# Kernel tuning notes

Measured on AMD Instinct MI355X. Metric: run time of the kernel, lower is better.

The kernel has to match this reference:

```python
import jax, jax.numpy as jnp
import numpy as np

B, SQ, SK, D = 8, 2048, 768, 768  # SK must equal D for layer_combine concat to typecheck


def setup_inputs() -> dict:
    key = jax.random.key(0)
    ks = jax.random.split(key, 13)
    s = 0.02
    return {
        "query": jax.random.normal(ks[0], (B, SQ, D), jnp.float32),
        "key_matrix": jax.random.normal(ks[1], (B, SK, D), jnp.float32),
        "value_matrix": jax.random.normal(ks[2], (B, SK, D), jnp.float32),
        "prev_layer": jax.random.normal(ks[3], (SK, D), jnp.float32) * s,
        "attention_mask": jax.random.randint(ks[4], (B, 1, SK), 0, 2, jnp.int32),
        "Wq": jax.random.normal(ks[5], (D, D), jnp.float32) * s,
        "bq": jax.random.normal(ks[6], (D,), jnp.float32) * s,
        "Wk": jax.random.normal(ks[7], (D, D), jnp.float32) * s,
        "bk": jax.random.normal(ks[8], (D,), jnp.float32) * s,
        "Wv": jax.random.normal(ks[9], (D, D), jnp.float32) * s,
        "bv": jax.random.normal(ks[10], (D,), jnp.float32) * s,
        "Wc": jax.random.normal(ks[11], (D, 2 * D), jnp.float32) * s,
        "bc": jax.random.normal(ks[12], (D,), jnp.float32) * s,
    }


def reference(query, key_matrix, value_matrix, prev_layer, attention_mask,
              Wq, bq, Wk, bk, Wv, bv, Wc, bc):
    # Linear projections (torch Linear: x @ W.T + b)
    Q = query @ Wq.T + bq                      # [B, SQ, D]
    K = key_matrix @ Wk.T + bk                 # [B, SK, D]
    V = value_matrix @ Wv.T + bv               # computed but unused when prev_layer given (faithful)
    scale = 1.0 / np.sqrt(D).astype(np.float32)
    scores = jnp.einsum('bqd,bkd->bqk', Q, K) * scale  # [B, SQ, SK]
    scores = jnp.where(attention_mask == 0, jnp.float32(-1e9), scores)
    # prev-layer integration: matmul + concat + linear combine
    layer_attn = scores @ prev_layer           # [B, SQ, D]
    combined = jnp.concatenate([scores, layer_attn], axis=-1)  # [B, SQ, 2D]
    out = combined @ Wc.T + bc                 # [B, SQ, D]
    return out
```

## Files before the change

### kernel.cpp

```cpp
#include <hip/hip_runtime.h>
#include <hip/hip_bf16.h>


typedef __attribute__((ext_vector_type(8))) short short8;
typedef __attribute__((ext_vector_type(4))) float f32x4;

#define SCALE 0.03608439182435161f

__device__ inline unsigned short f2bf(float x) {
  unsigned int u = __builtin_bit_cast(unsigned int, x);
  u = (u + 0x7fffu + ((u >> 16) & 1u)) >> 16;
  return (unsigned short)u;
}
__device__ inline float bf2f(unsigned short h) {
  return __builtin_bit_cast(float, ((unsigned int)h) << 16);
}

__global__ void k_cvt(const float* __restrict__ s, unsigned short* __restrict__ d, int n4) {
  int i = blockIdx.x * 256 + threadIdx.x;
  if (i >= n4) return;
  float4 v = reinterpret_cast<const float4*>(s)[i];
  reinterpret_cast<ushort4*>(d)[i] = make_ushort4(f2bf(v.x), f2bf(v.y), f2bf(v.z), f2bf(v.w));
}

__global__ void k_prep(const float* __restrict__ prev, const float* __restrict__ Wc,
                       unsigned short* __restrict__ prev_bf,
                       unsigned short* __restrict__ Wc2_bf) {
  int g = blockIdx.x;
  int region = g / 576;
  int idx = (g - region * 576) * 256 + threadIdx.x;
  float4 v;
  unsigned short* dst;
  if (region == 0) { v = reinterpret_cast<const float4*>(prev)[idx]; dst = prev_bf; }
  else {
    int r = idx / 192, c4 = (idx - r * 192) * 4;
    v = *reinterpret_cast<const float4*>(Wc + (long long)r * 1536 + 768 + c4);
    dst = Wc2_bf;
  }
  reinterpret_cast<ushort4*>(dst)[idx] = make_ushort4(f2bf(v.x), f2bf(v.y), f2bf(v.z), f2bf(v.w));
}

__global__ void k_tcvt(const float* __restrict__ Wq, const float* __restrict__ Wk,
                       const float* __restrict__ key, const int* __restrict__ mask,
                       unsigned short* __restrict__ WqT, unsigned short* __restrict__ WkT,
                       unsigned short* __restrict__ keyzT) {
  __shared__ float t[64][65];
  int z = blockIdx.z;
  const float* src;
  unsigned short* dst;
  const int* mb = nullptr;
  if (z == 0) { src = Wq; dst = WqT; }
  else if (z == 1) { src = Wk; dst = WkT; }
  else {
    int b = z - 2;
    src = key + (long long)b * 589824;
    dst = keyzT + (long long)b * 589824;
    mb = mask + b * 768;
  }
  int bx = blockIdx.x * 64, by = blockIdx.y * 64;
  int tx = threadIdx.x & 63, ty = threadIdx.x >> 6;
  #pragma unroll
  for (int i = 0; i < 64; i += 4) {
    float v = src[(long long)(by + ty + i) * 768 + bx + tx];
    if (mb) v = mb[by + ty + i] ? v : 0.0f;
    t[ty + i][tx] = v;
  }
  __syncthreads();
  #pragma unroll
  for (int i = 0; i < 64; i += 4)
    dst[(long long)(bx + ty + i) * 768 + by + tx] = f2bf(t[tx][ty + i]);
}

__global__ void k_sums(const unsigned short* __restrict__ WqT,
                       const unsigned short* __restrict__ WkT,
                       const float* __restrict__ bk, const float* __restrict__ bq,
                       const float* __restrict__ Mt, const int* __restrict__ mask,
                       float* __restrict__ u, float* __restrict__ w3,
                       float* __restrict__ s1, float* __restrict__ sm0) {
  int gw = blockIdx.x * 4 + (threadIdx.x >> 6);
  int lane = threadIdx.x & 63;
  if (gw < 1536) {
    const unsigned short* wrow = (gw < 768) ? (WqT + (long long)gw * 768)
                                            : (WkT + (long long)(gw - 768) * 768);
    const float* vec = (gw < 768) ? bk : bq;
    float s = 0.f;
    for (int j = lane; j < 768; j += 64) s += bf2f(wrow[j]) * vec[j];
    #pragma unroll
    for (int off = 32; off > 0; off >>= 1) s += __shfl_down(s, off, 64);
    if (lane == 0) { if (gw < 768) u[gw] = s; else w3[gw - 768] = s; }
  } else {
    int g2 = gw - 1536;
    int b = g2 / 768, d2 = g2 - b * 768;
    if (b >= 8) return;
    const int* mb = mask + b * 768;
    const float* mrow = Mt + (long long)d2 * 768;
    float a1 = 0.f, a0 = 0.f;
    for (int k = lane; k < 768; k += 64) {
      float v = mrow[k];
      if (mb[k]) a1 += v; else a0 += v;
    }
    #pragma unroll
    for (int off = 32; off > 0; off >>= 1) {
      a1 += __shfl_down(a1, off, 64);
      a0 += __shfl_down(a0, off, 64);
    }
    if (lane == 0) { s1[g2] = a1; sm0[g2] = a0; }
  }
}

__global__ void k_row(const unsigned short* __restrict__ Tt, const float* __restrict__ w3,
                      const float* __restrict__ s1, const float* __restrict__ sm0,
                      const float* __restrict__ bq, const float* __restrict__ bk,
                      const float* __restrict__ bc, float* __restrict__ row) {
  int gw = blockIdx.x * 4 + (threadIdx.x >> 6);
  int lane = threadIdx.x & 63;
  int b = gw / 768, d2 = gw - b * 768;
  if (b >= 8) return;
  const unsigned short* trow = Tt + ((long long)b * 768 + d2) * 768;
  float st = 0.f, sbb = 0.f;
  for (int j = lane; j < 768; j += 64) {
    st += bf2f(trow[j]) * w3[j];
    sbb += bq[j] * bk[j];
  }
  #pragma unroll
  for (int off = 32; off > 0; off >>= 1) {
    st += __shfl_down(st, off, 64);
    sbb += __shfl_down(sbb, off, 64);
  }
  if (lane == 0)
    row[gw] = bc[d2] - 1e9f * sm0[gw] + SCALE * (st + sbb * s1[gw]);
}

template <int MODE>
__global__ __launch_bounds__(256) void gemm_nt(
    const unsigned short* __restrict__ A, long long aStr, int lda,
    const unsigned short* __restrict__ B, long long bStr, int ldb,
    float* __restrict__ Cf, unsigned short* __restrict__ Cbf,
    long long cStr, int ldc,
    const float* __restrict__ aux, const float* __restrict__ aux2)
{
  constexpr int BM = 64, BN = 64, BK = 64;
  __shared__ __align__(16) char As[BM * BK * 2];
  __shared__ __align__(16) char Bs[BN * BK * 2];

  const int gx = gridDim.x, gy = gridDim.y;
  const int nwg = gx * gy * (int)gridDim.z;
  int lin = blockIdx.x + gx * (blockIdx.y + gy * blockIdx.z);
  int qq = nwg >> 3, rr = nwg & 7, xcd = lin & 7, loc = lin >> 3;
  int swz = (xcd < rr ? xcd * (qq + 1) : rr * (qq + 1) + (xcd - rr) * qq) + loc;
  int bz = swz / (gx * gy);
  int rem = swz - bz * gx * gy;
  int by = rem / gx, bx = rem - by * gx;

  const int b = bz;
  const unsigned short* Ab = A + (long long)b * aStr;
  const unsigned short* Bb = B + (long long)b * bStr;
  const int m0 = by * BM, n0 = bx * BN;

  const int tid = threadIdx.x;
  const int w = tid >> 6, lane = tid & 63;
  const int wr = w >> 1, wc = w & 1;
  const int fr = lane & 15, fq = lane >> 4;

  f32x4 acc[2][2] = {};

  for (int kt = 0; kt < 768; kt += BK) {
    __syncthreads();
    #pragma unroll
    for (int t = 0; t < 2; ++t) {
      int g = t * 256 + tid;
      int row = g >> 3, s = g & 7;
      int sg = (s - row) & 7;
      const unsigned short* ga = Ab + (long long)(m0 + row) * lda + kt + sg * 8;
      __builtin_amdgcn_global_load_lds(
          (const __attribute__((address_space(1))) void*)ga,
          (__attribute__((address_space(3))) void*)(As + g * 16), 16, 0, 0);
    }
    #pragma unroll
    for (int t = 0; t < 2; ++t) {
      int g = t * 256 + tid;
      int row = g >> 3, s = g & 7;
      int sg = (s - row) & 7;
      const unsigned short* gb = Bb + (long long)(n0 + row) * ldb + kt + sg * 8;
      __builtin_amdgcn_global_load_lds(
          (const __attribute__((address_space(1))) void*)gb,
          (__attribute__((address_space(3))) void*)(Bs + g * 16), 16, 0, 0);
    }
    __syncthreads();

    #pragma unroll
    for (int kk = 0; kk < 2; ++kk) {
      short8 af[2], bfr[2];
      #pragma unroll
      for (int i = 0; i < 2; ++i) {
        int r = wr * 32 + i * 16 + fr;
        int sgi = ((kk * 4 + fq) + r) & 7;
        af[i] = *reinterpret_cast<const short8*>(As + r * 128 + sgi * 16);
      }
      #pragma unroll
      for (int j = 0; j < 2; ++j) {
        int r = wc * 32 + j * 16 + fr;
        int sgj = ((kk * 4 + fq) + r) & 7;
        bfr[j] = *reinterpret_cast<const short8*>(Bs + r * 128 + sgj * 16);
      }
      #pragma unroll
      for (int i = 0; i < 2; ++i)
        #pragma unroll
        for (int j = 0; j < 2; ++j)
          acc[i][j] = __builtin_amdgcn_mfma_f32_16x16x32_bf16(af[i], bfr[j], acc[i][j], 0, 0, 0);
    }
  }

  #pragma unroll
  for (int i = 0; i < 2; ++i)
    #pragma unroll
    for (int j = 0; j < 2; ++j)
      #pragma unroll
      for (int r = 0; r < 4; ++r) {
        int row = m0 + wr * 32 + i * 16 + fq * 4 + r;
        int col = n0 + wc * 32 + j * 16 + fr;
        float v = acc[i][j][r];
        if constexpr (MODE == 0) {
          v += aux[(long long)row * 1536 + col];
          Cf[(long long)row * 768 + col] = v;
          Cbf[(long long)row * 768 + col] = f2bf(v);
        } else if constexpr (MODE == 2) {
          Cbf[(long long)b * cStr + (long long)row * ldc + col] = f2bf(v);
        } else {
          v += aux[b * 768 + row] * aux2[col];
          Cbf[(long long)b * cStr + (long long)row * ldc + col] = f2bf(v);
        }
      }
}

__global__ __launch_bounds__(512, 1) void g5_pipe(
    const unsigned short* __restrict__ A,
    const unsigned short* __restrict__ B,
    float* __restrict__ C, const float* __restrict__ rowv)
{
  __shared__ __align__(16) char As[2][256 * 128];
  __shared__ __align__(16) char Bs[2][192 * 128];

  int lin = blockIdx.x + 4 * (blockIdx.y + 8 * blockIdx.z);
  int swz = (lin & 7) * 32 + (lin >> 3);
  int bz = swz >> 5;
  int rem = swz & 31;
  int by = rem >> 2, bx = rem & 3;

  const int b = bz;
  const int m0 = by * 256, n0 = bx * 192;
  const unsigned short* Ab = A + (long long)b * 1572864;
  const unsigned short* Bb = B + (long long)b * 589824;

  const int tid = threadIdx.x;
  const int w = tid >> 6, lane = tid & 63;
  const int wr = w >> 2, wn = w & 3;
  const int fr = lane & 15, fq = lane >> 4;

  f32x4 acc[8][3] = {};

  auto stageA = [&](int buf, int kt, int s0, int ns) {
    for (int s = s0; s < s0 + ns; ++s) {
      int g = s * 512 + tid;
      int row = g >> 3, slot = g & 7;
      int sg = (slot - row) & 7;
      const unsigned short* ga = Ab + (long long)(m0 + row) * 768 + kt + sg * 8;
      __builtin_amdgcn_global_load_lds(
          (const __attribute__((address_space(1))) void*)ga,
          (__attribute__((address_space(3))) void*)(&As[buf][0] + g * 16), 16, 0, 0);
    }
  };
  auto stageB = [&](int buf, int kt, int s0, int ns) {
    for (int s = s0; s < s0 + ns; ++s) {
      int g = s * 512 + tid;
      int row = g >> 3, slot = g & 7;
      int sg = (slot - row) & 7;
      const unsigned short* gb = Bb + (long long)(n0 + row) * 768 + kt + sg * 8;
      __builtin_amdgcn_global_load_lds(
          (const __attribute__((address_space(1))) void*)gb,
          (__attribute__((address_space(3))) void*)(&Bs[buf][0] + g * 16), 16, 0, 0);
    }
  };

  stageA(0, 0, 0, 4);
  stageB(0, 0, 0, 3);
  asm volatile("s_waitcnt vmcnt(0)" ::: "memory");
  __builtin_amdgcn_s_barrier();
  __builtin_amdgcn_sched_barrier(0);

  int cur = 0;
  for (int t = 0; t < 12; ++t) {
    const char* as = &As[cur][0];
    const char* bs = &Bs[cur][0];
    const int ktn = (t + 1) * 64;
    short8 a0[4], a1[4], bb[3];

    #pragma unroll
    for (int i = 0; i < 4; ++i) {
      int r = wr * 128 + i * 16 + fr;
      a0[i] = *reinterpret_cast<const short8*>(as + r * 128 + (((fq) + r) & 7) * 16);
    }
    #pragma unroll
    for (int j = 0; j < 3; ++j) {
      int r = wn * 48 + j * 16 + fr;
      bb[j] = *reinterpret_cast<const short8*>(bs + r * 128 + (((fq) + r) & 7) * 16);
    }
    if (t < 11) stageA(cur ^ 1, ktn, 0, 2);
    __builtin_amdgcn_s_barrier();
    __builtin_amdgcn_s_setprio(1);
    #pragma unroll
    for (int i = 0; i < 4; ++i)
      #pragma unroll
      for (int j = 0; j < 3; ++j)
        acc[i][j] = __builtin_amdgcn_mfma_f32_16x16x32_bf16(a0[i], bb[j], acc[i][j], 0, 0, 0);
    __builtin_amdgcn_s_setprio(0);
    __builtin_amdgcn_s_barrier();

    #pragma unroll
    for (int i = 0; i < 4; ++i) {
      int r = wr * 128 + (4 + i) * 16 + fr;
      a1[i] = *reinterpret_cast<const short8*>(as + r * 128 + (((fq) + r) & 7) * 16);
    }
    if (t < 11) { stageA(cur ^ 1, ktn, 2, 2); stageB(cur ^ 1, ktn, 0, 1); }
    __builtin_amdgcn_s_barrier();
    __builtin_amdgcn_s_setprio(1);
    #pragma unroll
    for (int i = 0; i < 4; ++i)
      #pragma unroll
      for (int j = 0; j < 3; ++j)
        acc[4 + i][j] = __builtin_amdgcn_mfma_f32_16x16x32_bf16(a1[i], bb[j], acc[4 + i][j], 0, 0, 0);
    __builtin_amdgcn_s_setprio(0);
    __builtin_amdgcn_s_barrier();

    #pragma unroll
    for (int i = 0; i < 4; ++i) {
      int r = wr * 128 + i * 16 + fr;
      a0[i] = *reinterpret_cast<const short8*>(as + r * 128 + (((4 + fq) + r) & 7) * 16);
    }
    #pragma unroll
    for (int j = 0; j < 3; ++j) {
      int r = wn * 48 + j * 16 + fr;
      bb[j] = *reinterpret_cast<const short8*>(bs + r * 128 + (((4 + fq) + r) & 7) * 16);
    }
    if (t < 11) stageB(cur ^ 1, ktn, 1, 2);
    __builtin_amdgcn_s_barrier();
    __builtin_amdgcn_s_setprio(1);
    #pragma unroll
    for (int i = 0; i < 4; ++i)
      #pragma unroll
      for (int j = 0; j < 3; ++j)
        acc[i][j] = __builtin_amdgcn_mfma_f32_16x16x32_bf16(a0[i], bb[j], acc[i][j], 0, 0, 0);
    __builtin_amdgcn_s_setprio(0);
    __builtin_amdgcn_s_barrier();

    #pragma unroll
    for (int i = 0; i < 4; ++i) {
      int r = wr * 128 + (4 + i) * 16 + fr;
      a1[i] = *reinterpret_cast<const short8*>(as + r * 128 + (((4 + fq) + r) & 7) * 16);
    }
    __builtin_amdgcn_s_barrier();
    __builtin_amdgcn_s_setprio(1);
    #pragma unroll
    for (int i = 0; i < 4; ++i)
      #pragma unroll
      for (int j = 0; j < 3; ++j)
        acc[4 + i][j] = __builtin_amdgcn_mfma_f32_16x16x32_bf16(a1[i], bb[j], acc[4 + i][j], 0, 0, 0);
    __builtin_amdgcn_s_setprio(0);

    if (t < 11) asm volatile("s_waitcnt vmcnt(0)" ::: "memory");
    __builtin_amdgcn_s_barrier();
    cur ^= 1;
  }

  const long long ob = (long long)b * 1572864;
  #pragma unroll
  for (int i = 0; i < 8; ++i)
    #pragma unroll
    for (int j = 0; j < 3; ++j)
      #pragma unroll
      for (int r = 0; r < 4; ++r) {
        int row = m0 + wr * 128 + i * 16 + fq * 4 + r;
        int col = n0 + wn * 48 + j * 16 + fr;
        C[ob + (long long)row * 768 + col] = acc[i][j][r] * SCALE + rowv[b * 768 + col];
      }
}

extern "C" void kernel_launch(void* const* d_in, const int* in_sizes, int n_in,
                              void* d_out, int out_size, void* d_ws, size_t ws_size,
                              hipStream_t stream)
{
  const float* query = (const float*)d_in[0];
  const float* key   = (const float*)d_in[1];
  const float* prev  = (const float*)d_in[3];
  const int*   mask  = (const int*)d_in[4];
  const float* Wq    = (const float*)d_in[5];
  const float* bq    = (const float*)d_in[6];
  const float* Wk    = (const float*)d_in[7];
  const float* bk    = (const float*)d_in[8];
  const float* Wc    = (const float*)d_in[11];
  const float* bc    = (const float*)d_in[12];
  float* out = (float*)d_out;

  char* p = (char*)d_ws;
  size_t off = 0;
  auto alloc = [&](size_t bytes) {
    char* r = p + off;
    off += (bytes + 255) & ~(size_t)255;
    return r;
  };
  unsigned short* query_bf = (unsigned short*)alloc(12582912ull * 2);
  unsigned short* keyzT_bf = (unsigned short*)alloc(4718592ull * 2);
  unsigned short* WqT_bf   = (unsigned short*)alloc(589824ull * 2);
  unsigned short* WkT_bf   = (unsigned short*)alloc(589824ull * 2);
  unsigned short* prev_bf  = (unsigned short*)alloc(589824ull * 2);
  unsigned short* Wc2_bf   = (unsigned short*)alloc(589824ull * 2);
  float*          Mt_f     = (float*)alloc(589824ull * 4);
  unsigned short* Mt_bf    = (unsigned short*)alloc(589824ull * 2);
  unsigned short* W2_bf    = (unsigned short*)alloc(589824ull * 2);
  unsigned short* Tt_bf    = (unsigned short*)alloc(4718592ull * 2);
  unsigned short* Pt_bf    = (unsigned short*)alloc(4718592ull * 2);
  float*          s1f      = (float*)alloc(6144ull * 4);
  float*          sm0f     = (float*)alloc(6144ull * 4);
  float*          uv       = (float*)alloc(768ull * 4);
  float*          w3v      = (float*)alloc(768ull * 4);
  float*          rowv     = (float*)alloc(6144ull * 4);
  (void)ws_size; (void)in_sizes; (void)n_in; (void)out_size;

  k_cvt<<<dim3(12288), dim3(256), 0, stream>>>(query, query_bf, 3145728);
  k_tcvt<<<dim3(12, 12, 10), dim3(256), 0, stream>>>(Wq, Wk, key, mask,
                                                     WqT_bf, WkT_bf, keyzT_bf);
  k_prep<<<dim3(1152), dim3(256), 0, stream>>>(prev, Wc, prev_bf, Wc2_bf);

  gemm_nt<0><<<dim3(12, 12, 1), dim3(256), 0, stream>>>(
      Wc2_bf, 0ll, 768, prev_bf, 0ll, 768, Mt_f, Mt_bf, 0ll, 768,
      Wc, (const float*)nullptr);
  gemm_nt<2><<<dim3(12, 12, 1), dim3(256), 0, stream>>>(
      WqT_bf, 0ll, 768, WkT_bf, 0ll, 768, (float*)nullptr, W2_bf, 0ll, 768,
      (const float*)nullptr, (const float*)nullptr);
  k_sums<<<dim3(1920), dim3(256), 0, stream>>>(WqT_bf, WkT_bf, bk, bq, Mt_f, mask,
                                               uv, w3v, s1f, sm0f);
  gemm_nt<2><<<dim3(12, 12, 8), dim3(256), 0, stream>>>(
      Mt_bf, 0ll, 768, keyzT_bf, 589824ll, 768, (float*)nullptr, Tt_bf,
      589824ll, 768, (const float*)nullptr, (const float*)nullptr);
  gemm_nt<5><<<dim3(12, 12, 8), dim3(256), 0, stream>>>(
      Tt_bf, 589824ll, 768, W2_bf, 0ll, 768, (float*)nullptr, Pt_bf,
      589824ll, 768, s1f, uv);
  k_row<<<dim3(1536), dim3(256), 0, stream>>>(Tt_bf, w3v, s1f, sm0f, bq, bk, bc, rowv);
  g5_pipe<<<dim3(4, 8, 8), dim3(512), 0, stream>>>(query_bf, Pt_bf, out, rowv);
}
```

Measured before the change: 116.1 us.

## Triple-buffer A tiles in final GEMM and widen query conversion to 8 floats

The final pipelined GEMM now keeps three LDS buffers for the A tile and prefetches A two k-steps ahead, while B stays double-buffered one step ahead. It waits with vmcnt(4) instead of draining all loads at each iteration end, which lets the next A tile stay in flight during compute. The fp32-to-bf16 query conversion kernel also now handles 8 elements per thread with half the blocks. The extra A buffer raises LDS use to about 160KB per block, and the vmcnt counts depend on the exact number of outstanding loads being right.

Result: no change. 115.4 us (-0.6%).

```diff
diff --git a/kernel.cpp b/kernel.cpp
--- a/kernel.cpp
+++ b/kernel.cpp
@@ -16,11 +16,14 @@
   return __builtin_bit_cast(float, ((unsigned int)h) << 16);
 }
 
-__global__ void k_cvt(const float* __restrict__ s, unsigned short* __restrict__ d, int n4) {
+__global__ void k_cvt8(const float* __restrict__ s, unsigned short* __restrict__ d, int n8) {
   int i = blockIdx.x * 256 + threadIdx.x;
-  if (i >= n4) return;
-  float4 v = reinterpret_cast<const float4*>(s)[i];
-  reinterpret_cast<ushort4*>(d)[i] = make_ushort4(f2bf(v.x), f2bf(v.y), f2bf(v.z), f2bf(v.w));
+  if (i >= n8) return;
+  const float4* s4 = reinterpret_cast<const float4*>(s);
+  float4 v0 = s4[2 * i], v1 = s4[2 * i + 1];
+  ushort4* d4 = reinterpret_cast<ushort4*>(d);
+  d4[2 * i]     = make_ushort4(f2bf(v0.x), f2bf(v0.y), f2bf(v0.z), f2bf(v0.w));
+  d4[2 * i + 1] = make_ushort4(f2bf(v1.x), f2bf(v1.y), f2bf(v1.z), f2bf(v1.w));
 }
 
 __global__ void k_prep(const float* __restrict__ prev, const float* __restrict__ Wc,
@@ -238,7 +241,7 @@
     const unsigned short* __restrict__ B,
     float* __restrict__ C, const float* __restrict__ rowv)
 {
-  __shared__ __align__(16) char As[2][256 * 128];
+  __shared__ __align__(16) char As[3][256 * 128];
   __shared__ __align__(16) char Bs[2][192 * 128];
 
   int lin = blockIdx.x + 4 * (blockIdx.y + 8 * blockIdx.z);
@@ -284,15 +287,14 @@
 
   stageA(0, 0, 0, 4);
   stageB(0, 0, 0, 3);
-  asm volatile("s_waitcnt vmcnt(0)" ::: "memory");
+  stageA(1, 64, 0, 4);
+  asm volatile("s_waitcnt vmcnt(4)" ::: "memory");
   __builtin_amdgcn_s_barrier();
-  __builtin_amdgcn_sched_barrier(0);
-
-  int cur = 0;
+
   for (int t = 0; t < 12; ++t) {
-    const char* as = &As[cur][0];
-    const char* bs = &Bs[cur][0];
-    const int ktn = (t + 1) * 64;
+    const char* as = &As[t % 3][0];
+    const char* bs = &Bs[t & 1][0];
+    const int ktn1 = (t + 1) * 64, ktn2 = (t + 2) * 64;
     short8 a0[4], a1[4], bb[3];
 
     #pragma unroll
@@ -305,7 +307,7 @@
       int r = wn * 48 + j * 16 + fr;
       bb[j] = *reinterpret_cast<const short8*>(bs + r * 128 + (((fq) + r) & 7) * 16);
     }
-    if (t < 11) stageA(cur ^ 1, ktn, 0, 2);
+    if (t < 11) stageB((t + 1) & 1, ktn1, 0, 2);
     __builtin_amdgcn_s_barrier();
     __builtin_amdgcn_s_setprio(1);
     #pragma unroll
@@ -321,7 +323,8 @@
       int r = wr * 128 + (4 + i) * 16 + fr;
       a1[i] = *reinterpret_cast<const short8*>(as + r * 128 + (((fq) + r) & 7) * 16);
     }
-    if (t < 11) { stageA(cur ^ 1, ktn, 2, 2); stageB(cur ^ 1, ktn, 0, 1); }
+    if (t < 11) stageB((t + 1) & 1, ktn1, 2, 1);
+    if (t < 10) stageA((t + 2) % 3, ktn2, 0, 2);
     __builtin_amdgcn_s_barrier();
     __builtin_amdgcn_s_setprio(1);
     #pragma unroll
@@ -342,7 +345,7 @@
       int r = wn * 48 + j * 16 + fr;
       bb[j] = *reinterpret_cast<const short8*>(bs + r * 128 + (((4 + fq) + r) & 7) * 16);
     }
-    if (t < 11) stageB(cur ^ 1, ktn, 1, 2);
+    if (t < 10) stageA((t + 2) % 3, ktn2, 2, 2);
     __builtin_amdgcn_s_barrier();
     __builtin_amdgcn_s_setprio(1);
     #pragma unroll
@@ -367,9 +370,9 @@
         acc[4 + i][j] = __builtin_amdgcn_mfma_f32_16x16x32_bf16(a1[i], bb[j], acc[4 + i][j], 0, 0, 0);
     __builtin_amdgcn_s_setprio(0);
 
-    if (t < 11) asm volatile("s_waitcnt vmcnt(0)" ::: "memory");
-    __builtin_amdgcn_s_barrier();
-    cur ^= 1;
+    if (t < 10)       asm volatile("s_waitcnt vmcnt(4)" ::: "memory");
+    else if (t == 10) asm volatile("s_waitcnt vmcnt(0)" ::: "memory");
+    __builtin_amdgcn_s_barrier();
   }
 
   const long long ob = (long long)b * 1572864;
@@ -426,7 +429,7 @@
   float*          rowv     = (float*)alloc(6144ull * 4);
   (void)ws_size; (void)in_sizes; (void)n_in; (void)out_size;
 
-  k_cvt<<<dim3(12288), dim3(256), 0, stream>>>(query, query_bf, 3145728);
+  k_cvt8<<<dim3(6144), dim3(256), 0, stream>>>(query, query_bf, 1572864);
   k_tcvt<<<dim3(12, 12, 10), dim3(256), 0, stream>>>(Wq, Wk, key, mask,
                                                      WqT_bf, WkT_bf, keyzT_bf);
   k_prep<<<dim3(1152), dim3(256), 0, stream>>>(prev, Wc, prev_bf, Wc2_bf);
```
